# Kernel tuning notes

Measured on AMD Instinct MI355X. Metric: run time of the kernel, lower is better.

## Reference

```python
import jax, jax.numpy as jnp
import numpy as np

HIDDEN = 2048
VOCAB = 50257


def setup_inputs() -> dict:
    key = jax.random.key(0)
    ks = jax.random.split(key, 9)
    s = 1.0 / np.sqrt(HIDDEN)
    return {
        "input": jax.random.randint(ks[0], (1,), 0, VOCAB, dtype=jnp.int64) if jax.config.jax_enable_x64 else jax.random.randint(ks[0], (1,), 0, VOCAB, dtype=jnp.int32),
        "hidden": jax.random.normal(ks[1], (1, 1, HIDDEN), dtype=jnp.float32),
        "embedding": jax.random.normal(ks[2], (VOCAB, HIDDEN), dtype=jnp.float32),
        "w_ih": jax.random.uniform(ks[3], (3 * HIDDEN, HIDDEN), jnp.float32, -s, s),
        "w_hh": jax.random.uniform(ks[4], (3 * HIDDEN, HIDDEN), jnp.float32, -s, s),
        "b_ih": jax.random.uniform(ks[5], (3 * HIDDEN,), jnp.float32, -s, s),
        "b_hh": jax.random.uniform(ks[6], (3 * HIDDEN,), jnp.float32, -s, s),
        "out_w": jax.random.uniform(ks[7], (VOCAB, HIDDEN), jnp.float32, -s, s),
        "out_b": jax.random.uniform(ks[8], (VOCAB,), jnp.float32, -s, s),
    }


def reference(input, hidden, embedding, w_ih, w_hh, b_ih, b_hh, out_w, out_b):
    # embedding lookup + view(1,1,-1) + relu  -> x: [H]
    x = jax.nn.relu(embedding[input[0]])
    h = hidden[0, 0]  # [H]
    # PyTorch GRU single step: gates ordered (r, z, n)
    gi = w_ih @ x + b_ih  # [3H]
    gh = w_hh @ h + b_hh  # [3H]
    i_r, i_z, i_n = jnp.split(gi, 3)
    h_r, h_z, h_n = jnp.split(gh, 3)
    r = jax.nn.sigmoid(i_r + h_r)
    z = jax.nn.sigmoid(i_z + h_z)
    n = jnp.tanh(i_n + r * h_n)
    h_new = (1.0 - z) * n + z * h  # [H]
    # output projection (nn.Linear: x @ W.T + b) + log_softmax(dim=1)
    logits = out_w @ h_new + out_b  # [V]
    logp = jax.nn.log_softmax(logits)[None, :]  # [1, V]
    return logp, h_new[None, None, :]
```

## Files before the change

kernel.cpp:

```cpp
#include <hip/hip_runtime.h>
#include <math.h>

#define H 2048
#define V 50257
#define NTHR 256
#define LB 1024

typedef unsigned long long u64;

__device__ __forceinline__ float wave_reduce_sum(float v) {
#pragma unroll
    for (int off = 32; off > 0; off >>= 1)
        v += __shfl_down(v, off, 64);
    return v;
}

__device__ __forceinline__ void online_comb(float& m, float& s, float om, float os) {
    float M = fmaxf(m, om);
    s = s * __expf(m - M) + os * __expf(om - M);
    m = M;
}

__global__ __launch_bounds__(384) void k_gru(
    const int* __restrict__ idx_p, const float* __restrict__ emb,
    const float* __restrict__ hid,
    const float* __restrict__ w_ih, const float* __restrict__ w_hh,
    const float* __restrict__ b_ih, const float* __restrict__ b_hh,
    float* __restrict__ hnew_ws, float* __restrict__ hnew_out,
    u64* __restrict__ partials) {
    __shared__ float xs[H];
    __shared__ float hs[H];
    __shared__ float partial[6][2];
    int tid = threadIdx.x;

    if (tid == 0) partials[blockIdx.x] = 0ull;

    long idx = (long)idx_p[0];
    const float4* embrow = (const float4*)(emb + idx * (long)H);
    for (int i = tid; i < H / 4; i += 384) {
        float4 e = embrow[i];
        e.x = fmaxf(e.x, 0.f); e.y = fmaxf(e.y, 0.f);
        e.z = fmaxf(e.z, 0.f); e.w = fmaxf(e.w, 0.f);
        ((float4*)xs)[i] = e;
        ((float4*)hs)[i] = ((const float4*)hid)[i];
    }
    __syncthreads();

    int wid = tid >> 6, lane = tid & 63;
    int gate = wid % 3;
    const float* W   = (wid < 3) ? w_ih : w_hh;
    const float* vec = (wid < 3) ? xs : hs;
    int j0 = blockIdx.x, j1 = blockIdx.x + 1024;
    const float4* r0 = (const float4*)(W + ((size_t)gate * H + j0) * (size_t)H);
    const float4* r1 = (const float4*)(W + ((size_t)gate * H + j1) * (size_t)H);

    float4 vreg[8];
#pragma unroll
    for (int it = 0; it < 8; ++it)
        vreg[it] = ((const float4*)vec)[it * 64 + lane];

    float a0 = 0.f, a1 = 0.f;
#pragma unroll
    for (int it = 0; it < 8; ++it) {
        float4 wa = r0[it * 64 + lane];
        float4 wb = r1[it * 64 + lane];
        a0 += wa.x * vreg[it].x + wa.y * vreg[it].y + wa.z * vreg[it].z + wa.w * vreg[it].w;
        a1 += wb.x * vreg[it].x + wb.y * vreg[it].y + wb.z * vreg[it].z + wb.w * vreg[it].w;
    }
    a0 = wave_reduce_sum(a0);
    a1 = wave_reduce_sum(a1);
    if (lane == 0) { partial[wid][0] = a0; partial[wid][1] = a1; }
    __syncthreads();

    if (tid < 2) {
        int j = (tid == 0) ? j0 : j1;
        float i_r = partial[0][tid] + b_ih[j];
        float i_z = partial[1][tid] + b_ih[H + j];
        float i_n = partial[2][tid] + b_ih[2 * H + j];
        float h_r = partial[3][tid] + b_hh[j];
        float h_z = partial[4][tid] + b_hh[H + j];
        float h_n = partial[5][tid] + b_hh[2 * H + j];
        float r = 1.f / (1.f + expf(-(i_r + h_r)));
        float z = 1.f / (1.f + expf(-(i_z + h_z)));
        float n = tanhf(i_n + r * h_n);
        float hv = (1.f - z) * n + z * hs[j];
        hnew_ws[j] = hv;
        hnew_out[j] = hv;
    }
}

__global__ __launch_bounds__(NTHR, 4) void k_logits_fused(
    const float* __restrict__ out_w, const float* __restrict__ out_b,
    const float* __restrict__ hnew, float* __restrict__ out,
    u64* __restrict__ partials) {
    __shared__ float hsm[H];
    __shared__ float l_lds[4][13];
    __shared__ float pm[4], ps[4];
    __shared__ float c_s;
    const int tid = threadIdx.x, wid = tid >> 6, lane = tid & 63;
    const int gw = blockIdx.x * 4 + wid;

    for (int i = tid; i < H / 4; i += NTHR)
        ((float4*)hsm)[i] = ((const float4*)hnew)[i];
    __syncthreads();

    float4 vreg[8];
#pragma unroll
    for (int it = 0; it < 8; ++it)
        vreg[it] = ((const float4*)hsm)[it * 64 + lane];

    float m = -INFINITY, s = 0.f;
#pragma unroll 1
    for (int k = 0; k < 6; ++k) {
        int r0 = gw + (2 * k) * 4096;
        int r1 = r0 + 4096;
        const float4* row0 = (const float4*)(out_w + (size_t)r0 * H);
        const float4* row1 = (const float4*)(out_w + (size_t)r1 * H);
        float a0 = 0.f, a1 = 0.f;
#pragma unroll
        for (int it = 0; it < 8; ++it) {
            float4 wa = row0[it * 64 + lane];
            float4 wb = row1[it * 64 + lane];
            a0 += wa.x * vreg[it].x + wa.y * vreg[it].y + wa.z * vreg[it].z + wa.w * vreg[it].w;
            a1 += wb.x * vreg[it].x + wb.y * vreg[it].y + wb.z * vreg[it].z + wb.w * vreg[it].w;
        }
        a0 = wave_reduce_sum(a0);
        a1 = wave_reduce_sum(a1);
        if (lane == 0) {
            float l0 = a0 + out_b[r0], l1 = a1 + out_b[r1];
            l_lds[wid][2 * k]     = l0;
            l_lds[wid][2 * k + 1] = l1;
            online_comb(m, s, l0, 1.0f);
            online_comb(m, s, l1, 1.0f);
        }
    }
    const bool has_tail = gw < (V - 49152);
    if (has_tail) {
        int r = 49152 + gw;
        const float4* row = (const float4*)(out_w + (size_t)r * H);
        float a0 = 0.f;
#pragma unroll
        for (int it = 0; it < 8; ++it) {
            float4 wa = row[it * 64 + lane];
            a0 += wa.x * vreg[it].x + wa.y * vreg[it].y + wa.z * vreg[it].z + wa.w * vreg[it].w;
        }
        a0 = wave_reduce_sum(a0);
        if (lane == 0) {
            float l = a0 + out_b[r];
            l_lds[wid][12] = l;
            online_comb(m, s, l, 1.0f);
        }
    }
    if (lane == 0) { pm[wid] = m; ps[wid] = s; }
    __syncthreads();

    if (tid == 0) {
        float M = pm[0], S = ps[0];
        online_comb(M, S, pm[1], ps[1]);
        online_comb(M, S, pm[2], ps[2]);
        online_comb(M, S, pm[3], ps[3]);
        u64 pk = ((u64)__float_as_uint(S) << 32) | (u64)__float_as_uint(M);
        __hip_atomic_store(&partials[blockIdx.x], pk, __ATOMIC_RELAXED,
                           __HIP_MEMORY_SCOPE_AGENT);
    }

    float mm = -INFINITY, ss = 0.f;
    for (int i = tid; i < LB; i += NTHR) {
        u64 pk;
        while ((pk = __hip_atomic_load(&partials[i], __ATOMIC_RELAXED,
                                       __HIP_MEMORY_SCOPE_AGENT)) == 0ull)
            __builtin_amdgcn_s_sleep(8);
        float pmv = __uint_as_float((unsigned)(pk & 0xffffffffu));
        float psv = __uint_as_float((unsigned)(pk >> 32));
        online_comb(mm, ss, pmv, psv);
    }
#pragma unroll
    for (int off = 32; off > 0; off >>= 1) {
        float om = __shfl_down(mm, off, 64);
        float os = __shfl_down(ss, off, 64);
        online_comb(mm, ss, om, os);
    }
    if (lane == 0) { pm[wid] = mm; ps[wid] = ss; }
    __syncthreads();
    if (tid == 0) {
        float M = pm[0], S = ps[0];
        online_comb(M, S, pm[1], ps[1]);
        online_comb(M, S, pm[2], ps[2]);
        online_comb(M, S, pm[3], ps[3]);
        c_s = M + logf(S);
    }
    __syncthreads();
    const float C = c_s;

    if (lane < 12) {
        out[gw + lane * 4096] = l_lds[wid][lane] - C;
    } else if (lane == 12 && has_tail) {
        out[49152 + gw] = l_lds[wid][12] - C;
    }
}

extern "C" void kernel_launch(void* const* d_in, const int* in_sizes, int n_in,
                              void* d_out, int out_size, void* d_ws, size_t ws_size,
                              hipStream_t stream) {
    const int*   idx    = (const int*)d_in[0];
    const float* hidden = (const float*)d_in[1];
    const float* emb    = (const float*)d_in[2];
    const float* w_ih   = (const float*)d_in[3];
    const float* w_hh   = (const float*)d_in[4];
    const float* b_ih   = (const float*)d_in[5];
    const float* b_hh   = (const float*)d_in[6];
    const float* out_w  = (const float*)d_in[7];
    const float* out_b  = (const float*)d_in[8];

    float* out = (float*)d_out;
    float* ws  = (float*)d_ws;
    float* hnew     = ws;
    u64*   partials = (u64*)(ws + H);

    k_gru<<<1024, 384, 0, stream>>>(idx, emb, hidden, w_ih, w_hh, b_ih, b_hh,
                                    hnew, out + V, partials);
    k_logits_fused<<<LB, NTHR, 0, stream>>>(out_w, out_b, hnew, out, partials);
}
```

Before: 101.6 us.

## Pipeline output-projection rows through LDS with async global-to-LDS loads and fewer blocks

Halves the logits grid to 512 blocks so each wave handles 24-25 rows. Each row is streamed into double-buffered LDS slots with global_load_lds, with an explicit vmcnt wait, so the next row's load overlaps the current dot product. Biases are prefetched once per wave and broadcast with shuffles. Fewer blocks shorten the cross-block partial spin-wait, but the large LDS staging (64KB per block) limits occupancy, and the pipeline depth of two rows may not hide HBM latency as well as more resident waves did.

Measured after the change: 97.39 us (median of 2 runs). -4.2%, faster.

```diff
diff --git a/kernel.cpp b/kernel.cpp
--- a/kernel.cpp
+++ b/kernel.cpp
@@ -4,9 +4,21 @@
 #define H 2048
 #define V 50257
 #define NTHR 256
-#define LB 1024
+#define LB 512
+#define NW (LB * 4)
+#define ROWS_BASE 24
+#define TAIL (V - ROWS_BASE * NW)
 
 typedef unsigned long long u64;
+
+#if defined(__has_builtin)
+#if __has_builtin(__builtin_amdgcn_global_load_lds)
+#define HAS_GLL 1
+#endif
+#endif
+#ifndef HAS_GLL
+#define HAS_GLL 0
+#endif
 
 __device__ __forceinline__ float wave_reduce_sum(float v) {
 #pragma unroll
@@ -20,6 +32,14 @@
     s = s * __expf(m - M) + os * __expf(om - M);
     m = M;
 }
+
+#if HAS_GLL
+__device__ __forceinline__ void gl2lds16(const void* g, void* l) {
+    __builtin_amdgcn_global_load_lds(
+        (const __attribute__((address_space(1))) void*)g,
+        (__attribute__((address_space(3))) void*)l, 16, 0, 0);
+}
+#endif
 
 __global__ __launch_bounds__(384) void k_gru(
     const int* __restrict__ idx_p, const float* __restrict__ emb,
@@ -33,7 +53,7 @@
     __shared__ float partial[6][2];
     int tid = threadIdx.x;
 
-    if (tid == 0) partials[blockIdx.x] = 0ull;
+    if (tid == 0 && blockIdx.x < LB) partials[blockIdx.x] = 0ull;
 
     long idx = (long)idx_p[0];
     const float4* embrow = (const float4*)(emb + idx * (long)H);
@@ -89,19 +109,27 @@
     }
 }
 
-__global__ __launch_bounds__(NTHR, 4) void k_logits_fused(
+__global__ __launch_bounds__(NTHR, 2) void k_logits_fused(
     const float* __restrict__ out_w, const float* __restrict__ out_b,
     const float* __restrict__ hnew, float* __restrict__ out,
     u64* __restrict__ partials) {
     __shared__ float hsm[H];
-    __shared__ float l_lds[4][13];
+    __shared__ float stage[4][2][H];
+    __shared__ float l_lds[4][25];
     __shared__ float pm[4], ps[4];
     __shared__ float c_s;
     const int tid = threadIdx.x, wid = tid >> 6, lane = tid & 63;
     const int gw = blockIdx.x * 4 + wid;
+    const int nrows = ROWS_BASE + (gw < TAIL ? 1 : 0);
 
     for (int i = tid; i < H / 4; i += NTHR)
         ((float4*)hsm)[i] = ((const float4*)hnew)[i];
+    float bias = 0.f;
+    if (lane < nrows) {
+        int r = (lane < ROWS_BASE) ? (gw + lane * NW) : (ROWS_BASE * NW + gw);
+        bias = out_b[r];
+    }
+    asm volatile("" :: "v"(bias));
     __syncthreads();
 
     float4 vreg[8];
@@ -109,48 +137,68 @@
     for (int it = 0; it < 8; ++it)
         vreg[it] = ((const float4*)hsm)[it * 64 + lane];
 
+    float* slot0 = &stage[wid][0][0];
+    float* slot1 = &stage[wid][1][0];
+
     float m = -INFINITY, s = 0.f;
+
+#if HAS_GLL
+    auto issue_row = [&](int k) {
+        int r = (k < ROWS_BASE) ? (gw + k * NW) : (ROWS_BASE * NW + gw);
+        const char* gb = (const char*)(out_w + (size_t)r * H) + lane * 16;
+        char* lb = (char*)((k & 1) ? slot1 : slot0);
+#pragma unroll
+        for (int c = 0; c < 8; ++c)
+            gl2lds16(gb + c * 1024, lb + c * 1024);
+    };
+
+    issue_row(0);
+    issue_row(1);
 #pragma unroll 1
-    for (int k = 0; k < 6; ++k) {
-        int r0 = gw + (2 * k) * 4096;
-        int r1 = r0 + 4096;
-        const float4* row0 = (const float4*)(out_w + (size_t)r0 * H);
-        const float4* row1 = (const float4*)(out_w + (size_t)r1 * H);
-        float a0 = 0.f, a1 = 0.f;
+    for (int k = 0; k < nrows; ++k) {
+        if (k == nrows - 1) {
+            asm volatile("s_waitcnt vmcnt(0)" ::: "memory");
+        } else {
+            asm volatile("s_waitcnt vmcnt(8)" ::: "memory");
+        }
+        __builtin_amdgcn_sched_barrier(0);
+        const float4* s4 = (const float4*)((k & 1) ? slot1 : slot0);
+        float acc = 0.f;
 #pragma unroll
         for (int it = 0; it < 8; ++it) {
-            float4 wa = row0[it * 64 + lane];
-            float4 wb = row1[it * 64 + lane];
-            a0 += wa.x * vreg[it].x + wa.y * vreg[it].y + wa.z * vreg[it].z + wa.w * vreg[it].w;
-            a1 += wb.x * vreg[it].x + wb.y * vreg[it].y + wb.z * vreg[it].z + wb.w * vreg[it].w;
-        }
-        a0 = wave_reduce_sum(a0);
-        a1 = wave_reduce_sum(a1);
+            float4 w4 = s4[it * 64 + lane];
+            acc += w4.x * vreg[it].x + w4.y * vreg[it].y + w4.z * vreg[it].z + w4.w * vreg[it].w;
+        }
+        acc = wave_reduce_sum(acc);
+        float bk = __shfl(bias, k, 64);
         if (lane == 0) {
-            float l0 = a0 + out_b[r0], l1 = a1 + out_b[r1];
-            l_lds[wid][2 * k]     = l0;
-            l_lds[wid][2 * k + 1] = l1;
-            online_comb(m, s, l0, 1.0f);
-            online_comb(m, s, l1, 1.0f);
-        }
-    }
-    const bool has_tail = gw < (V - 49152);
-    if (has_tail) {
-        int r = 49152 + gw;
+            float l = acc + bk;
+            l_lds[wid][k] = l;
+            online_comb(m, s, l, 1.0f);
+        }
+        if (k + 2 < nrows) issue_row(k + 2);
+    }
+#else
+#pragma unroll 1
+    for (int k = 0; k < nrows; ++k) {
+        int r = (k < ROWS_BASE) ? (gw + k * NW) : (ROWS_BASE * NW + gw);
         const float4* row = (const float4*)(out_w + (size_t)r * H);
-        float a0 = 0.f;
+        float acc = 0.f;
 #pragma unroll
         for (int it = 0; it < 8; ++it) {
-            float4 wa = row[it * 64 + lane];
-            a0 += wa.x * vreg[it].x + wa.y * vreg[it].y + wa.z * vreg[it].z + wa.w * vreg[it].w;
-        }
-        a0 = wave_reduce_sum(a0);
+            float4 w4 = row[it * 64 + lane];
+            acc += w4.x * vreg[it].x + w4.y * vreg[it].y + w4.z * vreg[it].z + w4.w * vreg[it].w;
+        }
+        acc = wave_reduce_sum(acc);
+        float bk = __shfl(bias, k, 64);
         if (lane == 0) {
-            float l = a0 + out_b[r];
-            l_lds[wid][12] = l;
+            float l = acc + bk;
+            l_lds[wid][k] = l;
             online_comb(m, s, l, 1.0f);
         }
     }
+#endif
+
     if (lane == 0) { pm[wid] = m; ps[wid] = s; }
     __syncthreads();
 
@@ -163,6 +211,7 @@
         __hip_atomic_store(&partials[blockIdx.x], pk, __ATOMIC_RELAXED,
                            __HIP_MEMORY_SCOPE_AGENT);
     }
+    __syncthreads();
 
     float mm = -INFINITY, ss = 0.f;
     for (int i = tid; i < LB; i += NTHR) {
@@ -192,10 +241,10 @@
     __syncthreads();
     const float C = c_s;
 
-    if (lane < 12) {
-        out[gw + lane * 4096] = l_lds[wid][lane] - C;
-    } else if (lane == 12 && has_tail) {
-        out[49152 + gw] = l_lds[wid][12] - C;
+    if (lane < ROWS_BASE) {
+        out[gw + lane * NW] = l_lds[wid][lane] - C;
+    } else if (lane == ROWS_BASE && gw < TAIL) {
+        out[ROWS_BASE * NW + gw] = l_lds[wid][ROWS_BASE] - C;
     }
 }
 
```
